# Optimization experiments

Hardware: AMD Instinct MI355X
Metric: run time of the kernel (lower is better)

The kernel has to match this reference:

```python
import jax, jax.numpy as jnp
import numpy as np

D_MODEL = 512
D_AUX = 64
B, E = 8, 2048


def setup_inputs() -> dict:
    key = jax.random.key(0)
    ks = jax.random.split(key, 12)
    x = jax.random.normal(ks[0], (B, E, D_MODEL), dtype=jnp.float32)
    query_aux = jax.random.normal(ks[1], (B, E, D_AUX), dtype=jnp.float32)
    key_aux = jax.random.normal(ks[2], (B, E, D_AUX), dtype=jnp.float32)
    adjacency_mask = jax.random.randint(ks[3], (B, E, E), 0, 2, dtype=jnp.int32)
    merge_coefficients = jax.random.uniform(ks[4], (B, E, E), dtype=jnp.float32)
    # learned parameters of IrregularityAwareAttention (nn.Linear weights stored
    # as (out, in) in torch; we keep (in, out) for x @ W)
    s = 1.0 / np.sqrt(D_MODEL)
    Wq = jax.random.uniform(ks[5], (D_MODEL, D_MODEL), minval=-s, maxval=s, dtype=jnp.float32)
    bq = jax.random.uniform(ks[6], (D_MODEL,), minval=-s, maxval=s, dtype=jnp.float32)
    Wk = jax.random.uniform(ks[7], (D_MODEL, D_MODEL), minval=-s, maxval=s, dtype=jnp.float32)
    bk = jax.random.uniform(ks[8], (D_MODEL,), minval=-s, maxval=s, dtype=jnp.float32)
    Wv = jax.random.uniform(ks[9], (D_MODEL, D_MODEL), minval=-s, maxval=s, dtype=jnp.float32)
    bv = jax.random.uniform(ks[10], (D_MODEL,), minval=-s, maxval=s, dtype=jnp.float32)
    threshold = jnp.float32(0.5)
    return {
        "x": x, "query_aux": query_aux, "key_aux": key_aux,
        "adjacency_mask": adjacency_mask, "merge_coefficients": merge_coefficients,
        "Wq": Wq, "bq": bq, "Wk": Wk, "bk": bk, "Wv": Wv, "bv": bv,
        "threshold": threshold,
    }


def reference(x, query_aux, key_aux, adjacency_mask, merge_coefficients,
              Wq, bq, Wk, bk, Wv, bv, threshold):
    d_model = x.shape[-1]
    scale = jnp.asarray(d_model, x.dtype) ** 0.5
    q = x @ Wq + bq                      # (B, E, D)
    k = x @ Wk + bk
    v = x @ Wv + bv
    scores = jnp.einsum("bed,bfd->bef", q, k) / scale   # (B, E, E)

    aux_scale = jnp.asarray(key_aux.shape[-1], x.dtype) ** 0.5
    scores_aux = jnp.einsum("bed,bfd->bef", query_aux, key_aux) / aux_scale

    non_zero_mask = scores_aux != 0
    positive_mask = scores > threshold
    merge_mask = positive_mask & non_zero_mask
    blended = (1.0 - merge_coefficients) * scores + merge_coefficients * scores_aux
    scores = jnp.where(merge_mask, blended, scores)

    mask_value = jnp.finfo(scores.dtype).min
    scores = jnp.where(adjacency_mask == 0, mask_value, scores)

    attn = jax.nn.softmax(scores, axis=-1)
    return jnp.einsum("bef,bfd->bed", attn, v)
```

## Files before the change

### kernel.cpp

```cpp
#include <hip/hip_runtime.h>

#define E2 2048
#define DM 512

typedef __attribute__((ext_vector_type(8))) _Float16 half8;
typedef __attribute__((ext_vector_type(4))) _Float16 half4;
typedef __attribute__((ext_vector_type(8))) short short8;
typedef __attribute__((ext_vector_type(4))) short shortx4;
typedef __attribute__((ext_vector_type(4))) float floatx4;

__device__ __forceinline__ void stage_tile(const _Float16* __restrict__ g, int stride,
                                           _Float16* lds, int tid) {
  const int r0 = tid >> 2;
  const int c0 = (tid & 3) * 8;
  const int wbase = (tid >> 6) * 512;
#pragma unroll
  for (int h = 0; h < 2; ++h) {
    const _Float16* gp = g + (size_t)(h * 64 + r0) * stride + c0;
    _Float16* lp = lds + h * 2048 + wbase;
    __builtin_amdgcn_global_load_lds(
        (const __attribute__((address_space(1))) unsigned int*)gp,
        (__attribute__((address_space(3))) unsigned int*)lp, 16, 0, 0);
  }
}

__device__ __forceinline__ void mfma16(const _Float16* As, const _Float16* Bs,
                                       floatx4 acc[4][4], int wm, int wn, int lane) {
  const int m16 = lane & 15, quad = lane >> 4;
  half8 a[4];
#pragma unroll
  for (int i = 0; i < 4; ++i)
    a[i] = *(const half8*)(As + (wm * 64 + i * 16 + m16) * 32 + quad * 8);
#pragma unroll
  for (int j = 0; j < 4; ++j) {
    const half8 b = *(const half8*)(Bs + (wn * 64 + j * 16 + m16) * 32 + quad * 8);
#pragma unroll
    for (int i = 0; i < 4; ++i)
      acc[i][j] = __builtin_amdgcn_mfma_f32_16x16x32_f16(a[i], b, acc[i][j], 0, 0, 0);
  }
}

__device__ __forceinline__ void mfma48(const _Float16* Ah, const _Float16* Al,
                                       const _Float16* Bh, const _Float16* Bl,
                                       floatx4 acc[4][4], int wm, int wn, int lane) {
  const int m16 = lane & 15, quad = lane >> 4;
  half8 ah[4], al[4];
#pragma unroll
  for (int i = 0; i < 4; ++i) {
    const int off = (wm * 64 + i * 16 + m16) * 32 + quad * 8;
    ah[i] = *(const half8*)(Ah + off);
    al[i] = *(const half8*)(Al + off);
  }
#pragma unroll
  for (int j = 0; j < 4; ++j) {
    const int off = (wn * 64 + j * 16 + m16) * 32 + quad * 8;
    const half8 bh = *(const half8*)(Bh + off);
    const half8 bl = *(const half8*)(Bl + off);
#pragma unroll
    for (int i = 0; i < 4; ++i) {
      acc[i][j] = __builtin_amdgcn_mfma_f32_16x16x32_f16(ah[i], bh, acc[i][j], 0, 0, 0);
      acc[i][j] = __builtin_amdgcn_mfma_f32_16x16x32_f16(al[i], bh, acc[i][j], 0, 0, 0);
      acc[i][j] = __builtin_amdgcn_mfma_f32_16x16x32_f16(ah[i], bl, acc[i][j], 0, 0, 0);
    }
  }
}

__global__ void split_conv_k(const float* __restrict__ src, _Float16* __restrict__ hi,
                             _Float16* __restrict__ lo, float scale, int n8) {
  int i = blockIdx.x * blockDim.x + threadIdx.x;
  const int stride = gridDim.x * blockDim.x;
  const float4* s4 = (const float4*)src;
  for (; i < n8; i += stride) {
    const float4 u = s4[2 * i], v = s4[2 * i + 1];
    const float g[8] = {u.x, u.y, u.z, u.w, v.x, v.y, v.z, v.w};
    half8 h, l;
#pragma unroll
    for (int t = 0; t < 8; ++t) {
      const float gv = g[t] * scale;
      const _Float16 hv = (_Float16)gv;
      h[t] = hv;
      l[t] = (_Float16)(gv - (float)hv);
    }
    ((half8*)hi)[i] = h;
    ((half8*)lo)[i] = l;
  }
}

__global__ void conv_k(const float* __restrict__ src, _Float16* __restrict__ dst, int n8) {
  int i = blockIdx.x * blockDim.x + threadIdx.x;
  const int stride = gridDim.x * blockDim.x;
  const float4* s4 = (const float4*)src;
  for (; i < n8; i += stride) {
    const float4 u = s4[2 * i], v = s4[2 * i + 1];
    const float g[8] = {u.x, u.y, u.z, u.w, v.x, v.y, v.z, v.w};
    half8 h;
#pragma unroll
    for (int t = 0; t < 8; ++t) h[t] = (_Float16)g[t];
    ((half8*)dst)[i] = h;
  }
}

__global__ void transw_k(const float* __restrict__ Wq, const float* __restrict__ Wk,
                         const float* __restrict__ Wv, _Float16* __restrict__ Wth,
                         _Float16* __restrict__ Wtl) {
  const int z = blockIdx.z;
  const float* W = (z == 0) ? Wq : (z == 1) ? Wk : Wv;
  __shared__ float t[32][33];
  const int n0 = blockIdx.x * 32, k0 = blockIdx.y * 32;
  const int tx = threadIdx.x, ty = threadIdx.y;
#pragma unroll
  for (int i = 0; i < 32; i += 8) t[ty + i][tx] = W[(size_t)(k0 + ty + i) * DM + n0 + tx];
  __syncthreads();
  const size_t zb = (size_t)z * DM * DM;
#pragma unroll
  for (int i = 0; i < 32; i += 8) {
    const float g = t[tx][ty + i] * 64.0f;
    const _Float16 h = (_Float16)g;
    const size_t o = zb + (size_t)(n0 + ty + i) * DM + (k0 + tx);
    Wth[o] = h;
    Wtl[o] = (_Float16)(g - (float)h);
  }
}

__global__ __launch_bounds__(256, 2) void qkv_k(
    const _Float16* __restrict__ xh, const _Float16* __restrict__ xl,
    const _Float16* __restrict__ Wth, const _Float16* __restrict__ Wtl,
    const float* __restrict__ bqp, const float* __restrict__ bkp,
    const float* __restrict__ bvp,
    _Float16* __restrict__ qh, _Float16* __restrict__ ql,
    _Float16* __restrict__ kh, _Float16* __restrict__ kl,
    _Float16* __restrict__ vT) {
  __shared__ _Float16 Ah[2][4096], Al[2][4096], Bh[2][4096], Bl[2][4096];
  const int tid = threadIdx.x, lane = tid & 63, wv = tid >> 6;
  const int wm = wv >> 1, wn = wv & 1;
  const int bm = blockIdx.x, bn = blockIdx.y, z = blockIdx.z;
  const bool split = (z < 2);
  const _Float16* Ash = xh + (size_t)bm * 128 * DM;
  const _Float16* Asl = xl + (size_t)bm * 128 * DM;
  const _Float16* Bsh = Wth + ((size_t)z * DM + bn * 128) * DM;
  const _Float16* Bsl = Wtl + ((size_t)z * DM + bn * 128) * DM;
  floatx4 acc[4][4];
  const floatx4 z4 = {0.f, 0.f, 0.f, 0.f};
#pragma unroll
  for (int i = 0; i < 4; ++i)
#pragma unroll
    for (int j = 0; j < 4; ++j) acc[i][j] = z4;

  stage_tile(Ash, DM, Ah[0], tid);
  stage_tile(Bsh, DM, Bh[0], tid);
  if (split) { stage_tile(Asl, DM, Al[0], tid); stage_tile(Bsl, DM, Bl[0], tid); }
  __syncthreads();
  for (int kt = 0; kt < 16; ++kt) {
    const int cur = kt & 1, nxt = cur ^ 1;
    if (kt < 15) {
      const int ko = (kt + 1) * 32;
      stage_tile(Ash + ko, DM, Ah[nxt], tid);
      stage_tile(Bsh + ko, DM, Bh[nxt], tid);
      if (split) { stage_tile(Asl + ko, DM, Al[nxt], tid); stage_tile(Bsl + ko, DM, Bl[nxt], tid); }
    }
    if (split) mfma48(Ah[cur], Al[cur], Bh[cur], Bl[cur], acc, wm, wn, lane);
    else       mfma16(Ah[cur], Bh[cur], acc, wm, wn, lane);
    __syncthreads();
  }
  const int m16 = lane & 15, quad = lane >> 4;
  const float* bias = (z == 0) ? bqp : (z == 1) ? bkp : bvp;
  if (split) {
    _Float16* oh = (z == 0) ? qh : kh;
    _Float16* ol = (z == 0) ? ql : kl;
#pragma unroll
    for (int j = 0; j < 4; ++j) {
      const int n = bn * 128 + wn * 64 + j * 16 + m16;
      const float bb = bias[n];
#pragma unroll
      for (int i = 0; i < 4; ++i) {
        const int m = bm * 128 + wm * 64 + i * 16 + quad * 4;
#pragma unroll
        for (int r = 0; r < 4; ++r) {
          const float val = acc[i][j][r] * (1.0f / 256.0f) + bb;
          const float v8 = val * 8.0f;
          const _Float16 h = (_Float16)v8;
          const _Float16 l = (_Float16)(v8 - (float)h);
          const size_t o = (size_t)(m + r) * DM + n;
          oh[o] = h; ol[o] = l;
        }
      }
    }
  } else {
#pragma unroll
    for (int j = 0; j < 4; ++j) {
      const int n = bn * 128 + wn * 64 + j * 16 + m16;
      const float bb = bias[n];
#pragma unroll
      for (int i = 0; i < 4; ++i) {
        const int m = bm * 128 + wm * 64 + i * 16 + quad * 4;
        const int bidx = m >> 11, e0 = m & 2047;
        half4 pk;
#pragma unroll
        for (int r = 0; r < 4; ++r)
          pk[r] = (_Float16)(acc[i][j][r] * (1.0f / 256.0f) + bb);
        *(half4*)(vT + ((size_t)bidx * DM + n) * E2 + e0) = pk;
      }
    }
  }
}

__global__ __launch_bounds__(256, 2) void scores_k(
    const _Float16* __restrict__ qh, const _Float16* __restrict__ ql,
    const _Float16* __restrict__ kh, const _Float16* __restrict__ kl,
    const _Float16* __restrict__ qah, const _Float16* __restrict__ kah,
    const int* __restrict__ adj, const float* __restrict__ mc,
    const float* __restrict__ thrp, unsigned short* __restrict__ sc) {
  __shared__ _Float16 S[32768];
  _Float16* const AhB = S;
  _Float16* const AlB = S + 8192;
  _Float16* const BhB = S + 16384;
  _Float16* const BlB = S + 24576;
  const int tid = threadIdx.x, lane = tid & 63, wv = tid >> 6;
  const int wm = wv >> 1, wn = wv & 1;
  const int bf = blockIdx.x, be = blockIdx.y, b = blockIdx.z;
  const _Float16* Ash = qh + ((size_t)b * E2 + be * 128) * DM;
  const _Float16* Asl = ql + ((size_t)b * E2 + be * 128) * DM;
  const _Float16* Bsh = kh + ((size_t)b * E2 + bf * 128) * DM;
  const _Float16* Bsl = kl + ((size_t)b * E2 + bf * 128) * DM;
  floatx4 accm[4][4];
  const floatx4 z4 = {0.f, 0.f, 0.f, 0.f};
#pragma unroll
  for (int i = 0; i < 4; ++i)
#pragma unroll
    for (int j = 0; j < 4; ++j) accm[i][j] = z4;

  stage_tile(Ash, DM, AhB, tid);
  stage_tile(Bsh, DM, BhB, tid);
  stage_tile(Asl, DM, AlB, tid);
  stage_tile(Bsl, DM, BlB, tid);
  __syncthreads();
  for (int kt = 0; kt < 16; ++kt) {
    const int cur = kt & 1, nxt = cur ^ 1;
    if (kt < 15) {
      const int ko = (kt + 1) * 32;
      stage_tile(Ash + ko, DM, AhB + nxt * 4096, tid);
      stage_tile(Bsh + ko, DM, BhB + nxt * 4096, tid);
      stage_tile(Asl + ko, DM, AlB + nxt * 4096, tid);
      stage_tile(Bsl + ko, DM, BlB + nxt * 4096, tid);
    }
    mfma48(AhB + cur * 4096, AlB + cur * 4096, BhB + cur * 4096, BlB + cur * 4096,
           accm, wm, wn, lane);
    __syncthreads();
  }
  floatx4 acca[4][4];
#pragma unroll
  for (int i = 0; i < 4; ++i)
#pragma unroll
    for (int j = 0; j < 4; ++j) acca[i][j] = z4;
  const _Float16* A2 = qah + ((size_t)b * E2 + be * 128) * 64;
  const _Float16* B2 = kah + ((size_t)b * E2 + bf * 128) * 64;
  stage_tile(A2, 64, AhB, tid);
  stage_tile(B2, 64, BhB, tid);
  stage_tile(A2 + 32, 64, AhB + 4096, tid);
  stage_tile(B2 + 32, 64, BhB + 4096, tid);
  __syncthreads();
  mfma16(AhB, BhB, acca, wm, wn, lane);
  mfma16(AhB + 4096, BhB + 4096, acca, wm, wn, lane);

  float* const sL = (float*)S;
  _Float16* const saL = S + 16384;
  const float thr = *thrp;
  const int m16 = lane & 15, quad = lane >> 4;
#pragma unroll
  for (int h = 0; h < 2; ++h) {
    __syncthreads();
    if (wm == h) {
#pragma unroll
      for (int j = 0; j < 4; ++j) {
        const int cl = wn * 64 + j * 16 + m16;
#pragma unroll
        for (int i = 0; i < 4; ++i) {
#pragma unroll
          for (int r = 0; r < 4; ++r) {
            const int rl = i * 16 + quad * 4 + r;
            sL[rl * 128 + cl] = accm[i][j][r] * (0.015625f * 0.044194173824159216f);
            saL[rl * 128 + cl] = (_Float16)(acca[i][j][r] * 0.125f);
          }
        }
      }
    }
    __syncthreads();
    const size_t rowbase = (size_t)b * E2 + be * 128 + h * 64;
#pragma unroll
    for (int g = 0; g < 8; ++g) {
      const int tf = g * 1024 + tid * 4;
      const int rl = tf >> 7, cl = tf & 127;
      const size_t idx = (rowbase + rl) * E2 + bf * 128 + cl;
      const int4 a4 = *(const int4*)(adj + idx);
      const float4 c4 = *(const float4*)(mc + idx);
      const float4 s4v = *(const float4*)(sL + rl * 128 + cl);
      const half4 sa4 = *(const half4*)(saL + rl * 128 + cl);
      const float ss[4] = {s4v.x, s4v.y, s4v.z, s4v.w};
      const int aa[4] = {a4.x, a4.y, a4.z, a4.w};
      const float cc[4] = {c4.x, c4.y, c4.z, c4.w};
      shortx4 o;
#pragma unroll
      for (int t = 0; t < 4; ++t) {
        float s = ss[t];
        const float sa = (float)sa4[t];
        if (sa != 0.0f && s > thr) s = (1.0f - cc[t]) * s + cc[t] * sa;
        unsigned short ov;
        if (aa[t] == 0) {
          ov = 0xFBFFu;
        } else {
          union { _Float16 hh; unsigned short u; } u;
          u.hh = (_Float16)s;
          ov = u.u;
        }
        o[t] = (short)ov;
      }
      *(shortx4*)(sc + idx) = o;
    }
  }
}

__global__ __launch_bounds__(256) void softmax_k(unsigned short* __restrict__ sc) {
  const size_t row = blockIdx.x;
  unsigned short* p = sc + row * E2;
  const int tid = threadIdx.x, lane = tid & 63, wv = tid >> 6;
  const short8 raw = *(const short8*)(p + tid * 8);
  float f[8];
#pragma unroll
  for (int t = 0; t < 8; ++t) {
    union { _Float16 h; short s; } u; u.s = raw[t];
    f[t] = (float)u.h;
  }
  float mx = f[0];
#pragma unroll
  for (int t = 1; t < 8; ++t) mx = fmaxf(mx, f[t]);
#pragma unroll
  for (int o = 32; o > 0; o >>= 1) mx = fmaxf(mx, __shfl_xor(mx, o, 64));
  __shared__ float red[8];
  if (lane == 0) red[wv] = mx;
  __syncthreads();
  mx = fmaxf(fmaxf(red[0], red[1]), fmaxf(red[2], red[3]));
  float ef[8], sum = 0.f;
#pragma unroll
  for (int t = 0; t < 8; ++t) { ef[t] = __expf(f[t] - mx); sum += ef[t]; }
#pragma unroll
  for (int o = 32; o > 0; o >>= 1) sum += __shfl_xor(sum, o, 64);
  if (lane == 0) red[4 + wv] = sum;
  __syncthreads();
  sum = (red[4] + red[5]) + (red[6] + red[7]);
  const float inv = 1.0f / sum;
  short8 ov;
#pragma unroll
  for (int t = 0; t < 8; ++t) {
    union { _Float16 h; short s; } u;
    u.h = (_Float16)(ef[t] * inv);
    ov[t] = u.s;
  }
  *(short8*)(p + tid * 8) = ov;
}

__global__ __launch_bounds__(256, 2) void pv_k(
    const _Float16* __restrict__ at, const _Float16* __restrict__ vT,
    float* __restrict__ out) {
  __shared__ _Float16 As[2][4096], Bs[2][4096];
  const int tid = threadIdx.x, lane = tid & 63, wv = tid >> 6;
  const int wm = wv >> 1, wn = wv & 1;
  const int bd = blockIdx.x, be = blockIdx.y, b = blockIdx.z;
  const _Float16* Asrc = at + ((size_t)b * E2 + be * 128) * E2;
  const _Float16* Bsrc = vT + ((size_t)b * DM + bd * 128) * E2;
  floatx4 acc[4][4];
  const floatx4 z4 = {0.f, 0.f, 0.f, 0.f};
#pragma unroll
  for (int i = 0; i < 4; ++i)
#pragma unroll
    for (int j = 0; j < 4; ++j) acc[i][j] = z4;
  stage_tile(Asrc, E2, As[0], tid);
  stage_tile(Bsrc, E2, Bs[0], tid);
  __syncthreads();
  for (int kt = 0; kt < 64; ++kt) {
    const int cur = kt & 1, nxt = cur ^ 1;
    if (kt < 63) {
      const int ko = (kt + 1) * 32;
      stage_tile(Asrc + ko, E2, As[nxt], tid);
      stage_tile(Bsrc + ko, E2, Bs[nxt], tid);
    }
    mfma16(As[cur], Bs[cur], acc, wm, wn, lane);
    __syncthreads();
  }
  const int m16 = lane & 15, quad = lane >> 4;
#pragma unroll
  for (int j = 0; j < 4; ++j) {
    const int d = bd * 128 + wn * 64 + j * 16 + m16;
#pragma unroll
    for (int i = 0; i < 4; ++i) {
      const int e0 = be * 128 + wm * 64 + i * 16 + quad * 4;
#pragma unroll
      for (int r = 0; r < 4; ++r)
        out[((size_t)b * E2 + e0 + r) * DM + d] = acc[i][j][r];
    }
  }
}

extern "C" void kernel_launch(void* const* d_in, const int* in_sizes, int n_in,
                              void* d_out, int out_size, void* d_ws, size_t ws_size,
                              hipStream_t stream) {
  const float* x   = (const float*)d_in[0];
  const float* qa  = (const float*)d_in[1];
  const float* ka  = (const float*)d_in[2];
  const int*   adj = (const int*)d_in[3];
  const float* mc  = (const float*)d_in[4];
  const float* Wq  = (const float*)d_in[5];
  const float* bq  = (const float*)d_in[6];
  const float* Wk  = (const float*)d_in[7];
  const float* bk  = (const float*)d_in[8];
  const float* Wv  = (const float*)d_in[9];
  const float* bv  = (const float*)d_in[10];
  const float* thr = (const float*)d_in[11];
  float* out = (float*)d_out;
  char* w = (char*)d_ws;
  const size_t MiB = 1ull << 20;
  _Float16* xh  = (_Float16*)(w + 0 * MiB);
  _Float16* xl  = (_Float16*)(w + 16 * MiB);
  _Float16* qhp = (_Float16*)(w + 32 * MiB);
  _Float16* qlp = (_Float16*)(w + 48 * MiB);
  _Float16* khp = (_Float16*)(w + 64 * MiB);
  _Float16* klp = (_Float16*)(w + 80 * MiB);
  _Float16* vT  = (_Float16*)(w + 96 * MiB);
  _Float16* Wth = (_Float16*)(w + 112 * MiB);
  _Float16* Wtl = (_Float16*)(w + 114 * MiB);
  _Float16* qah = (_Float16*)(w + 116 * MiB);
  _Float16* kah = (_Float16*)(w + 118 * MiB);
  unsigned short* sc = (unsigned short*)(w + 120 * MiB);

  split_conv_k<<<2048, 256, 0, stream>>>(x, xh, xl, 4.0f, (8 * E2 * DM) / 8);
  conv_k<<<256, 256, 0, stream>>>(qa, qah, (8 * E2 * 64) / 8);
  conv_k<<<256, 256, 0, stream>>>(ka, kah, (8 * E2 * 64) / 8);
  transw_k<<<dim3(16, 16, 3), dim3(32, 8), 0, stream>>>(Wq, Wk, Wv, Wth, Wtl);
  qkv_k<<<dim3(128, 4, 3), 256, 0, stream>>>(xh, xl, Wth, Wtl, bq, bk, bv,
                                             qhp, qlp, khp, klp, vT);
  scores_k<<<dim3(16, 16, 8), 256, 0, stream>>>(qhp, qlp, khp, klp, qah, kah,
                                                adj, mc, thr, sc);
  softmax_k<<<16384, 256, 0, stream>>>(sc);
  pv_k<<<dim3(4, 16, 8), 256, 0, stream>>>((const _Float16*)sc, vT, out);
}
```

Before: 606.0 us.

## Use 8 waves per block in qkv and scores GEMMs, halving per-wave tiles

The qkv and scores kernels now launch 512 threads (8 waves, a 2x4 wave grid) instead of 256, so each wave owns a 64x32 sub-tile. The accumulator count per wave halves, and tile staging is reworked so each thread issues one LDS-direct load per tile. The scores epilogue LDS staging now uses a padded row stride of 132 to reduce bank conflicts. The aim is more waves in flight to hide memory and MFMA latency, at the cost of lower register reuse of the A fragments per wave.

```diff
diff --git a/kernel.cpp b/kernel.cpp
--- a/kernel.cpp
+++ b/kernel.cpp
@@ -24,6 +24,17 @@
   }
 }
 
+__device__ __forceinline__ void stage_tile8(const _Float16* __restrict__ g, int stride,
+                                            _Float16* lds, int tid) {
+  const int r0 = tid >> 2;
+  const int c0 = (tid & 3) * 8;
+  const int wbase = (tid >> 6) * 512;
+  const _Float16* gp = g + (size_t)r0 * stride + c0;
+  __builtin_amdgcn_global_load_lds(
+      (const __attribute__((address_space(1))) unsigned int*)gp,
+      (__attribute__((address_space(3))) unsigned int*)(lds + wbase), 16, 0, 0);
+}
+
 __device__ __forceinline__ void mfma16(const _Float16* As, const _Float16* Bs,
                                        floatx4 acc[4][4], int wm, int wn, int lane) {
   const int m16 = lane & 15, quad = lane >> 4;
@@ -40,9 +51,25 @@
   }
 }
 
-__device__ __forceinline__ void mfma48(const _Float16* Ah, const _Float16* Al,
+__device__ __forceinline__ void mfma8(const _Float16* As, const _Float16* Bs,
+                                      floatx4 acc[4][2], int wm, int wn, int lane) {
+  const int m16 = lane & 15, quad = lane >> 4;
+  half8 a[4];
+#pragma unroll
+  for (int i = 0; i < 4; ++i)
+    a[i] = *(const half8*)(As + (wm * 64 + i * 16 + m16) * 32 + quad * 8);
+#pragma unroll
+  for (int j = 0; j < 2; ++j) {
+    const half8 b = *(const half8*)(Bs + (wn * 32 + j * 16 + m16) * 32 + quad * 8);
+#pragma unroll
+    for (int i = 0; i < 4; ++i)
+      acc[i][j] = __builtin_amdgcn_mfma_f32_16x16x32_f16(a[i], b, acc[i][j], 0, 0, 0);
+  }
+}
+
+__device__ __forceinline__ void mfma24(const _Float16* Ah, const _Float16* Al,
                                        const _Float16* Bh, const _Float16* Bl,
-                                       floatx4 acc[4][4], int wm, int wn, int lane) {
+                                       floatx4 acc[4][2], int wm, int wn, int lane) {
   const int m16 = lane & 15, quad = lane >> 4;
   half8 ah[4], al[4];
 #pragma unroll
@@ -52,8 +79,8 @@
     al[i] = *(const half8*)(Al + off);
   }
 #pragma unroll
-  for (int j = 0; j < 4; ++j) {
-    const int off = (wn * 64 + j * 16 + m16) * 32 + quad * 8;
+  for (int j = 0; j < 2; ++j) {
+    const int off = (wn * 32 + j * 16 + m16) * 32 + quad * 8;
     const half8 bh = *(const half8*)(Bh + off);
     const half8 bl = *(const half8*)(Bl + off);
 #pragma unroll
@@ -122,7 +149,7 @@
   }
 }
 
-__global__ __launch_bounds__(256, 2) void qkv_k(
+__global__ __launch_bounds__(512, 4) void qkv_k(
     const _Float16* __restrict__ xh, const _Float16* __restrict__ xl,
     const _Float16* __restrict__ Wth, const _Float16* __restrict__ Wtl,
     const float* __restrict__ bqp, const float* __restrict__ bkp,
@@ -132,34 +159,34 @@
     _Float16* __restrict__ vT) {
   __shared__ _Float16 Ah[2][4096], Al[2][4096], Bh[2][4096], Bl[2][4096];
   const int tid = threadIdx.x, lane = tid & 63, wv = tid >> 6;
-  const int wm = wv >> 1, wn = wv & 1;
+  const int wm = wv >> 2, wn = wv & 3;
   const int bm = blockIdx.x, bn = blockIdx.y, z = blockIdx.z;
   const bool split = (z < 2);
   const _Float16* Ash = xh + (size_t)bm * 128 * DM;
   const _Float16* Asl = xl + (size_t)bm * 128 * DM;
   const _Float16* Bsh = Wth + ((size_t)z * DM + bn * 128) * DM;
   const _Float16* Bsl = Wtl + ((size_t)z * DM + bn * 128) * DM;
-  floatx4 acc[4][4];
+  floatx4 acc[4][2];
   const floatx4 z4 = {0.f, 0.f, 0.f, 0.f};
 #pragma unroll
   for (int i = 0; i < 4; ++i)
 #pragma unroll
-    for (int j = 0; j < 4; ++j) acc[i][j] = z4;
-
-  stage_tile(Ash, DM, Ah[0], tid);
-  stage_tile(Bsh, DM, Bh[0], tid);
-  if (split) { stage_tile(Asl, DM, Al[0], tid); stage_tile(Bsl, DM, Bl[0], tid); }
+    for (int j = 0; j < 2; ++j) acc[i][j] = z4;
+
+  stage_tile8(Ash, DM, Ah[0], tid);
+  stage_tile8(Bsh, DM, Bh[0], tid);
+  if (split) { stage_tile8(Asl, DM, Al[0], tid); stage_tile8(Bsl, DM, Bl[0], tid); }
   __syncthreads();
   for (int kt = 0; kt < 16; ++kt) {
     const int cur = kt & 1, nxt = cur ^ 1;
     if (kt < 15) {
       const int ko = (kt + 1) * 32;
-      stage_tile(Ash + ko, DM, Ah[nxt], tid);
-      stage_tile(Bsh + ko, DM, Bh[nxt], tid);
-      if (split) { stage_tile(Asl + ko, DM, Al[nxt], tid); stage_tile(Bsl + ko, DM, Bl[nxt], tid); }
-    }
-    if (split) mfma48(Ah[cur], Al[cur], Bh[cur], Bl[cur], acc, wm, wn, lane);
-    else       mfma16(Ah[cur], Bh[cur], acc, wm, wn, lane);
+      stage_tile8(Ash + ko, DM, Ah[nxt], tid);
+      stage_tile8(Bsh + ko, DM, Bh[nxt], tid);
+      if (split) { stage_tile8(Asl + ko, DM, Al[nxt], tid); stage_tile8(Bsl + ko, DM, Bl[nxt], tid); }
+    }
+    if (split) mfma24(Ah[cur], Al[cur], Bh[cur], Bl[cur], acc, wm, wn, lane);
+    else       mfma8(Ah[cur], Bh[cur], acc, wm, wn, lane);
     __syncthreads();
   }
   const int m16 = lane & 15, quad = lane >> 4;
@@ -168,8 +195,8 @@
     _Float16* oh = (z == 0) ? qh : kh;
     _Float16* ol = (z == 0) ? ql : kl;
 #pragma unroll
-    for (int j = 0; j < 4; ++j) {
-      const int n = bn * 128 + wn * 64 + j * 16 + m16;
+    for (int j = 0; j < 2; ++j) {
+      const int n = bn * 128 + wn * 32 + j * 16 + m16;
       const float bb = bias[n];
 #pragma unroll
       for (int i = 0; i < 4; ++i) {
@@ -187,8 +214,8 @@
     }
   } else {
 #pragma unroll
-    for (int j = 0; j < 4; ++j) {
-      const int n = bn * 128 + wn * 64 + j * 16 + m16;
+    for (int j = 0; j < 2; ++j) {
+      const int n = bn * 128 + wn * 32 + j * 16 + m16;
       const float bb = bias[n];
 #pragma unroll
       for (int i = 0; i < 4; ++i) {
@@ -204,7 +231,7 @@
   }
 }
 
-__global__ __launch_bounds__(256, 2) void scores_k(
+__global__ __launch_bounds__(512, 4) void scores_k(
     const _Float16* __restrict__ qh, const _Float16* __restrict__ ql,
     const _Float16* __restrict__ kh, const _Float16* __restrict__ kl,
     const _Float16* __restrict__ qah, const _Float16* __restrict__ kah,
@@ -216,54 +243,54 @@
   _Float16* const BhB = S + 16384;
   _Float16* const BlB = S + 24576;
   const int tid = threadIdx.x, lane = tid & 63, wv = tid >> 6;
-  const int wm = wv >> 1, wn = wv & 1;
+  const int wm = wv >> 2, wn = wv & 3;
   const int bf = blockIdx.x, be = blockIdx.y, b = blockIdx.z;
   const _Float16* Ash = qh + ((size_t)b * E2 + be * 128) * DM;
   const _Float16* Asl = ql + ((size_t)b * E2 + be * 128) * DM;
   const _Float16* Bsh = kh + ((size_t)b * E2 + bf * 128) * DM;
   const _Float16* Bsl = kl + ((size_t)b * E2 + bf * 128) * DM;
-  floatx4 accm[4][4];
+  floatx4 accm[4][2];
   const floatx4 z4 = {0.f, 0.f, 0.f, 0.f};
 #pragma unroll
   for (int i = 0; i < 4; ++i)
 #pragma unroll
-    for (int j = 0; j < 4; ++j) accm[i][j] = z4;
-
-  stage_tile(Ash, DM, AhB, tid);
-  stage_tile(Bsh, DM, BhB, tid);
-  stage_tile(Asl, DM, AlB, tid);
-  stage_tile(Bsl, DM, BlB, tid);
+    for (int j = 0; j < 2; ++j) accm[i][j] = z4;
+
+  stage_tile8(Ash, DM, AhB, tid);
+  stage_tile8(Bsh, DM, BhB, tid);
+  stage_tile8(Asl, DM, AlB, tid);
+  stage_tile8(Bsl, DM, BlB, tid);
   __syncthreads();
   for (int kt = 0; kt < 16; ++kt) {
     const int cur = kt & 1, nxt = cur ^ 1;
     if (kt < 15) {
       const int ko = (kt + 1) * 32;
-      stage_tile(Ash + ko, DM, AhB + nxt * 4096, tid);
-      stage_tile(Bsh + ko, DM, BhB + nxt * 4096, tid);
-      stage_tile(Asl + ko, DM, AlB + nxt * 4096, tid);
-      stage_tile(Bsl + ko, DM, BlB + nxt * 4096, tid);
-    }
-    mfma48(AhB + cur * 4096, AlB + cur * 4096, BhB + cur * 4096, BlB + cur * 4096,
+      stage_tile8(Ash + ko, DM, AhB + nxt * 4096, tid);
+      stage_tile8(Bsh + ko, DM, BhB + nxt * 4096, tid);
+      stage_tile8(Asl + ko, DM, AlB + nxt * 4096, tid);
+      stage_tile8(Bsl + ko, DM, BlB + nxt * 4096, tid);
+    }
+    mfma24(AhB + cur * 4096, AlB + cur * 4096, BhB + cur * 4096, BlB + cur * 4096,
            accm, wm, wn, lane);
     __syncthreads();
   }
-  floatx4 acca[4][4];
-#pragma unroll
-  for (int i = 0; i < 4; ++i)
-#pragma unroll
-    for (int j = 0; j < 4; ++j) acca[i][j] = z4;
+  floatx4 acca[4][2];
+#pragma unroll
+  for (int i = 0; i < 4; ++i)
+#pragma unroll
+    for (int j = 0; j < 2; ++j) acca[i][j] = z4;
   const _Float16* A2 = qah + ((size_t)b * E2 + be * 128) * 64;
   const _Float16* B2 = kah + ((size_t)b * E2 + bf * 128) * 64;
-  stage_tile(A2, 64, AhB, tid);
-  stage_tile(B2, 64, BhB, tid);
-  stage_tile(A2 + 32, 64, AhB + 4096, tid);
-  stage_tile(B2 + 32, 64, BhB + 4096, tid);
-  __syncthreads();
-  mfma16(AhB, BhB, acca, wm, wn, lane);
-  mfma16(AhB + 4096, BhB + 4096, acca, wm, wn, lane);
+  stage_tile8(A2, 64, AhB, tid);
+  stage_tile8(B2, 64, BhB, tid);
+  stage_tile8(A2 + 32, 64, AhB + 4096, tid);
+  stage_tile8(B2 + 32, 64, BhB + 4096, tid);
+  __syncthreads();
+  mfma8(AhB, BhB, acca, wm, wn, lane);
+  mfma8(AhB + 4096, BhB + 4096, acca, wm, wn, lane);
 
   float* const sL = (float*)S;
-  _Float16* const saL = S + 16384;
+  _Float16* const saL = S + 16896;
   const float thr = *thrp;
   const int m16 = lane & 15, quad = lane >> 4;
 #pragma unroll
@@ -271,15 +298,15 @@
     __syncthreads();
     if (wm == h) {
 #pragma unroll
-      for (int j = 0; j < 4; ++j) {
-        const int cl = wn * 64 + j * 16 + m16;
+      for (int j = 0; j < 2; ++j) {
+        const int cl = wn * 32 + j * 16 + m16;
 #pragma unroll
         for (int i = 0; i < 4; ++i) {
 #pragma unroll
           for (int r = 0; r < 4; ++r) {
             const int rl = i * 16 + quad * 4 + r;
-            sL[rl * 128 + cl] = accm[i][j][r] * (0.015625f * 0.044194173824159216f);
-            saL[rl * 128 + cl] = (_Float16)(acca[i][j][r] * 0.125f);
+            sL[rl * 132 + cl] = accm[i][j][r] * (0.015625f * 0.044194173824159216f);
+            saL[rl * 132 + cl] = (_Float16)(acca[i][j][r] * 0.125f);
           }
         }
       }
@@ -287,14 +314,14 @@
     __syncthreads();
     const size_t rowbase = (size_t)b * E2 + be * 128 + h * 64;
 #pragma unroll
-    for (int g = 0; g < 8; ++g) {
-      const int tf = g * 1024 + tid * 4;
+    for (int g = 0; g < 4; ++g) {
+      const int tf = g * 2048 + tid * 4;
       const int rl = tf >> 7, cl = tf & 127;
       const size_t idx = (rowbase + rl) * E2 + bf * 128 + cl;
       const int4 a4 = *(const int4*)(adj + idx);
       const float4 c4 = *(const float4*)(mc + idx);
-      const float4 s4v = *(const float4*)(sL + rl * 128 + cl);
-      const half4 sa4 = *(const half4*)(saL + rl * 128 + cl);
+      const float4 s4v = *(const float4*)(sL + rl * 132 + cl);
+      const half4 sa4 = *(const half4*)(saL + rl * 132 + cl);
       const float ss[4] = {s4v.x, s4v.y, s4v.z, s4v.w};
       const int aa[4] = {a4.x, a4.y, a4.z, a4.w};
       const float cc[4] = {c4.x, c4.y, c4.z, c4.w};
@@ -435,9 +462,9 @@
   conv_k<<<256, 256, 0, stream>>>(qa, qah, (8 * E2 * 64) / 8);
   conv_k<<<256, 256, 0, stream>>>(ka, kah, (8 * E2 * 64) / 8);
   transw_k<<<dim3(16, 16, 3), dim3(32, 8), 0, stream>>>(Wq, Wk, Wv, Wth, Wtl);
-  qkv_k<<<dim3(128, 4, 3), 256, 0, stream>>>(xh, xl, Wth, Wtl, bq, bk, bv,
+  qkv_k<<<dim3(128, 4, 3), 512, 0, stream>>>(xh, xl, Wth, Wtl, bq, bk, bv,
                                              qhp, qlp, khp, klp, vT);
-  scores_k<<<dim3(16, 16, 8), 256, 0, stream>>>(qhp, qlp, khp, klp, qah, kah,
+  scores_k<<<dim3(16, 16, 8), 512, 0, stream>>>(qhp, qlp, khp, klp, qah, kah,
                                                 adj, mc, thr, sc);
   softmax_k<<<16384, 256, 0, stream>>>(sc);
   pv_k<<<dim3(4, 16, 8), 256, 0, stream>>>((const _Float16*)sc, vT, out);
```

Result: faster. 580.0 us (-4.3%).
